# Kernel optimization log

Hardware: AMD Instinct MI355X
Metric: run time of the kernel (lower is better)

## Reference

```python
import jax, jax.numpy as jnp
import numpy as np

NEG_INF = -9e15
LEAKY_SLOPE = 0.2  # init alpha
N, IN_DIM, OUT_DIM = 8192, 512, 256


def setup_inputs() -> dict:
    key = jax.random.key(0)
    k1, k2, k3, k4, k5 = jax.random.split(key, 5)
    h = jax.random.normal(k1, (N, IN_DIM), dtype=jnp.float32)
    adj = jax.random.randint(k2, (N, N), 0, 2, dtype=jnp.int32)
    W = jax.random.normal(k3, (IN_DIM, OUT_DIM), dtype=jnp.float32) * 0.06
    a_left = jax.random.normal(k4, (OUT_DIM, 1), dtype=jnp.float32) * 0.1
    a_right = jax.random.normal(k5, (OUT_DIM, 1), dtype=jnp.float32) * 0.1
    return {"h": h, "adj": adj, "W": W, "a_left": a_left, "a_right": a_right}


def reference(h, adj, W, a_left, a_right):
    Wh = h @ W                                  # [N, out_dim]
    Wh1 = Wh @ a_left                           # [N, 1]
    Wh2 = Wh @ a_right                          # [N, 1]
    e = Wh1 + Wh2.T                             # [N, N] broadcast additive scores
    e = jnp.where(e > 0, e, LEAKY_SLOPE * e)    # LeakyReLU
    e = jnp.where(adj > 0, e, NEG_INF)          # adjacency mask
    attention = jax.nn.softmax(e, axis=1)       # row-wise softmax (dropout=0, eval)
    h_out = attention @ Wh                      # [N, out_dim]
    return jax.nn.elu(h_out)                    # activation=True
```

## Files before the change

kernel.cpp:

```cpp
#include <hip/hip_runtime.h>
#include <hip/hip_bf16.h>
#include <cstdint>
#include <cstddef>

typedef float  f32x4  __attribute__((ext_vector_type(4)));
typedef __bf16 bf16x8 __attribute__((ext_vector_type(8)));

#define LOG2E 1.4426950408889634f

static constexpr int GN   = 8192;
static constexpr int GIN  = 512;
static constexpr int GOUT = 256;

static __device__ __forceinline__ void gload_lds16(const void* g, void* lds){
  typedef uint32_t __attribute__((address_space(1)))* gp_t;
  typedef uint32_t __attribute__((address_space(3)))* lp_t;
  __builtin_amdgcn_global_load_lds((gp_t)(uintptr_t)g,
                                   (lp_t)(uint32_t)(uintptr_t)lds, 16, 0, 0);
}

__global__ __launch_bounds__(256) void k_pre1(const float* __restrict__ W,
                                              const float* __restrict__ al,
                                              const float* __restrict__ ar,
                                              const float* __restrict__ h,
                                              float* __restrict__ wal,
                                              float* __restrict__ war,
                                              __bf16* __restrict__ WT,
                                              __bf16* __restrict__ hb){
  __shared__ float T[64][65];
  const int bid = blockIdx.x, tid = threadIdx.x;
  if(bid < 128){
    const int k = bid*4 + (tid>>6), lane = tid & 63;
    float4 wv = ((const float4*)(W + (size_t)k*GOUT))[lane];
    float4 av = ((const float4*)al)[lane];
    float4 bv = ((const float4*)ar)[lane];
    float sl = wv.x*av.x + wv.y*av.y + wv.z*av.z + wv.w*av.w;
    float sr = wv.x*bv.x + wv.y*bv.y + wv.z*bv.z + wv.w*bv.w;
    #pragma unroll
    for(int o=32;o;o>>=1){ sl += __shfl_down(sl,o,64); sr += __shfl_down(sr,o,64); }
    if(lane==0){ wal[k] = sl*LOG2E; war[k] = sr*LOG2E; }
  } else if(bid < 160){
    const int tile = bid - 128;
    const int k0 = (tile>>2)*64, c0 = (tile&3)*64;
    const int r = tid>>2, cs = (tid&3)*16;
    #pragma unroll
    for(int j=0;j<4;j++){
      float4 v = *(const float4*)(W + (size_t)(k0+r)*GOUT + c0 + cs + 4*j);
      T[r][cs+4*j+0]=v.x; T[r][cs+4*j+1]=v.y; T[r][cs+4*j+2]=v.z; T[r][cs+4*j+3]=v.w;
    }
    __syncthreads();
    bf16x8 o1, o2;
    #pragma unroll
    for(int j=0;j<8;j++){ o1[j]=(__bf16)T[cs+j][r]; o2[j]=(__bf16)T[cs+8+j][r]; }
    __bf16* dst = WT + (size_t)(c0+r)*GIN + k0 + cs;
    *(bf16x8*)dst = o1;
    *(bf16x8*)(dst+8) = o2;
  } else {
    size_t i = ((size_t)(bid-160)*256 + tid)*8;
    float4 v0 = *(const float4*)(h+i);
    float4 v1 = *(const float4*)(h+i+4);
    bf16x8 o;
    o[0]=(__bf16)v0.x; o[1]=(__bf16)v0.y; o[2]=(__bf16)v0.z; o[3]=(__bf16)v0.w;
    o[4]=(__bf16)v1.x; o[5]=(__bf16)v1.y; o[6]=(__bf16)v1.z; o[7]=(__bf16)v1.w;
    *(bf16x8*)(hb+i) = o;
  }
}

__global__ __launch_bounds__(256) void k_pre2(const int* __restrict__ adj,
                                              unsigned int* __restrict__ pk,
                                              const __bf16* __restrict__ WT,
                                              const __bf16* __restrict__ hb,
                                              __bf16* __restrict__ WhbT,
                                              const float* __restrict__ h,
                                              const float* __restrict__ wal,
                                              const float* __restrict__ war,
                                              float* __restrict__ Wh1,
                                              float* __restrict__ Wh2){
  __shared__ __attribute__((aligned(16))) __bf16 As[2][64*64];
  __shared__ __attribute__((aligned(16))) __bf16 Bs[2][128*64];
  const int bid = blockIdx.x, tid = threadIdx.x;
  const int lane = tid & 63, w = tid >> 6;

  if(bid < 2048){
    const int Wv = bid*4 + w;
    const int jb = Wv & 127;
    const int g  = Wv >> 7;
    const size_t cb = (size_t)jb*64 + lane;
    const int idx = lane & 15;
    #pragma unroll 1
    for(int i=0;i<8;i++){
      const int r0 = (g*8 + i)*16;
      int a[16];
      #pragma unroll
      for(int r=0;r<16;r++) a[r] = adj[(size_t)(r0+r)*GN + cb];
      uint64_t b0 = __ballot(a[0]!=0),  b1 = __ballot(a[1]!=0);
      uint64_t b2 = __ballot(a[2]!=0),  b3 = __ballot(a[3]!=0);
      uint64_t b4 = __ballot(a[4]!=0),  b5 = __ballot(a[5]!=0);
      uint64_t b6 = __ballot(a[6]!=0),  b7 = __ballot(a[7]!=0);
      uint64_t b8 = __ballot(a[8]!=0),  b9 = __ballot(a[9]!=0);
      uint64_t bA = __ballot(a[10]!=0), bB = __ballot(a[11]!=0);
      uint64_t bC = __ballot(a[12]!=0), bD = __ballot(a[13]!=0);
      uint64_t bE = __ballot(a[14]!=0), bF = __ballot(a[15]!=0);
      uint64_t c0 = (idx&1)? b1:b0, c1 = (idx&1)? b3:b2;
      uint64_t c2 = (idx&1)? b5:b4, c3 = (idx&1)? b7:b6;
      uint64_t c4 = (idx&1)? b9:b8, c5 = (idx&1)? bB:bA;
      uint64_t c6 = (idx&1)? bD:bC, c7 = (idx&1)? bF:bE;
      uint64_t d0 = (idx&2)? c1:c0, d1 = (idx&2)? c3:c2;
      uint64_t d2 = (idx&2)? c5:c4, d3 = (idx&2)? c7:c6;
      uint64_t e0 = (idx&4)? d1:d0, e1 = (idx&4)? d3:d2;
      uint64_t v  = (idx&8)? e1:e0;
      unsigned int hword = (lane&16)? (unsigned int)(v>>32) : (unsigned int)v;
      if(lane < 32){
        pk[(size_t)(2*jb + (lane>>4))*GN + r0 + idx] = hword;
      }
    }
  } else if(bid < 2304){
    const int b2 = bid - 2048;
    const int mb = b2 >> 6, nb = b2 & 63;
    const int m0 = mb*64, n0 = nb*128;

    f32x4 acc[8];
    #pragma unroll
    for(int t=0;t<8;t++) acc[t] = (f32x4){0.f,0.f,0.f,0.f};

    const int lr = lane>>3;
    const int bs_sw = ((lane&7)*16) ^ (lr<<4);

    auto stage = [&](int it, int buf){
      const int k0b = it*128;
      #pragma unroll
      for(int s=0;s<6;s++){
        int u = w + s*4;
        const char* src; char* dst;
        if(u < 8){
          int r8 = u*8;
          src = (const char*)(WT + (size_t)(m0 + r8 + lr)*GIN);
          dst = (char*)&As[buf][0] + r8*128;
        } else {
          int r8 = (u-8)*8;
          src = (const char*)(hb + (size_t)(n0 + r8 + lr)*GIN);
          dst = (char*)&Bs[buf][0] + r8*128;
        }
        gload_lds16(src + k0b + bs_sw, dst);
      }
    };

    auto kstep = [&](int kk, int buf){
      const int ko = kk*64 + (lane>>4)*16;
      const int am = 16*w + (lane&15);
      bf16x8 af = *(const bf16x8*)((const char*)&As[buf][0] + am*128 + (ko ^ ((am&7)<<4)));
      #pragma unroll
      for(int t=0;t<8;t++){
        int n = 16*t + (lane&15);
        bf16x8 bf = *(const bf16x8*)((const char*)&Bs[buf][0] + n*128 + (ko ^ ((n&7)<<4)));
        acc[t] = __builtin_amdgcn_mfma_f32_16x16x32_bf16(af, bf, acc[t], 0, 0, 0);
      }
    };

    stage(0,0);
    asm volatile("s_waitcnt vmcnt(0)" ::: "memory");
    __builtin_amdgcn_s_barrier();
    for(int it=0; it<8; it++){
      int buf = it & 1;
      if(it < 7) stage(it+1, buf^1);
      kstep(0, buf);
      kstep(1, buf);
      asm volatile("s_waitcnt vmcnt(0)" ::: "memory");
      __builtin_amdgcn_s_barrier();
    }

    const int mrow = m0 + 16*w + 4*(lane>>4);
    const int nc0  = n0 + (lane&15);
    #pragma unroll
    for(int t=0;t<8;t++){
      #pragma unroll
      for(int r=0;r<4;r++){
        WhbT[(size_t)(mrow + r)*GN + nc0 + 16*t] = (__bf16)acc[t][r];
      }
    }
  } else {
    const int row = (bid-2304)*4 + w;
    const float4* hp = (const float4*)(h + (size_t)row*GIN);
    float4 v0 = hp[lane*2], v1 = hp[lane*2+1];
    float4 a0 = ((const float4*)wal)[lane*2], a1 = ((const float4*)wal)[lane*2+1];
    float4 b0 = ((const float4*)war)[lane*2], b1 = ((const float4*)war)[lane*2+1];
    float sl = v0.x*a0.x+v0.y*a0.y+v0.z*a0.z+v0.w*a0.w
             + v1.x*a1.x+v1.y*a1.y+v1.z*a1.z+v1.w*a1.w;
    float sr = v0.x*b0.x+v0.y*b0.y+v0.z*b0.z+v0.w*b0.w
             + v1.x*b1.x+v1.y*b1.y+v1.z*b1.z+v1.w*b1.w;
    #pragma unroll
    for(int of=32;of;of>>=1){ sl += __shfl_down(sl,of,64); sr += __shfl_down(sr,of,64); }
    if(lane==0){ Wh1[row]=sl; Wh2[row]=sr; }
  }
}

template<bool PART>
__global__ __launch_bounds__(256,2) void k_attn(const unsigned int* __restrict__ pk,
                                                const __bf16* __restrict__ WhbT,
                                                const float* __restrict__ Wh1s,
                                                const float* __restrict__ Wh2s,
                                                float* __restrict__ pv_out,
                                                float* __restrict__ s_out){
  __shared__ __attribute__((aligned(16))) char Vs[3][16384];
  const int tid = threadIdx.x, lane = tid & 63, w = tid >> 6;
  const int rg = blockIdx.x >> 3, chunk = blockIdx.x & 7;
  const int r0 = rg * 128;
  const int j0 = chunk * 1024;
  const int la = lane & 15, kg = lane >> 4, kg8 = kg << 3;

  f32x4 acc0[16], acc1[16];
  #pragma unroll
  for(int t=0;t<16;t++){ acc0[t] = (f32x4){0.f,0.f,0.f,0.f}; acc1[t] = (f32x4){0.f,0.f,0.f,0.f}; }
  f32x4 accs0 = (f32x4){0.f,0.f,0.f,0.f};
  f32x4 accs1 = (f32x4){0.f,0.f,0.f,0.f};

  bf16x8 ones;
  #pragma unroll
  for(int j=0;j<8;j++) ones[j] = (__bf16)1.0f;

  const int myrow0 = r0 + 16*w + la;
  const float wh1_0 = Wh1s[myrow0];
  const float wh1_1 = Wh1s[myrow0 + 64];

  const unsigned int* pkb = pk + (size_t)(chunk*32)*GN + r0 + 16*w + la;

  const int l_log = (lane&7) ^ (lane>>3);
  const char* wbase = (const char*)WhbT
                    + (size_t)(64*w + 2*(lane>>3) + (l_log>>2))*(GN*2)
                    + (size_t)(l_log&3)*16;

  auto stage = [&](int it, int buf){
    const size_t colb = (size_t)(j0 + it*32)*2;
    char* dst = &Vs[buf][0] + w*4096 + lane*16;
    #pragma unroll
    for(int s=0;s<4;s++){
      gload_lds16(wbase + (size_t)(16*s)*(GN*2) + colb, dst + s*1024);
    }
  };

  unsigned int mr0, mr1, nr0, nr1;
  auto mload = [&](int it, unsigned int& a, unsigned int& b){
    a = pkb[(size_t)it*GN];
    b = pkb[(size_t)it*GN + 64];
  };

  auto mkpa = [&](float wh1, unsigned m8, float4 w0, float4 w1) -> bf16x8 {
    bf16x8 pa;
    float y, p;
    y = wh1 + w0.x; y = fmaxf(y, 0.2f*y); p = exp2f(y); pa[0] = (__bf16)((m8    )&1 ? p : 0.f);
    y = wh1 + w0.y; y = fmaxf(y, 0.2f*y); p = exp2f(y); pa[1] = (__bf16)((m8>>1)&1 ? p : 0.f);
    y = wh1 + w0.z; y = fmaxf(y, 0.2f*y); p = exp2f(y); pa[2] = (__bf16)((m8>>2)&1 ? p : 0.f);
    y = wh1 + w0.w; y = fmaxf(y, 0.2f*y); p = exp2f(y); pa[3] = (__bf16)((m8>>3)&1 ? p : 0.f);
    y = wh1 + w1.x; y = fmaxf(y, 0.2f*y); p = exp2f(y); pa[4] = (__bf16)((m8>>4)&1 ? p : 0.f);
    y = wh1 + w1.y; y = fmaxf(y, 0.2f*y); p = exp2f(y); pa[5] = (__bf16)((m8>>5)&1 ? p : 0.f);
    y = wh1 + w1.z; y = fmaxf(y, 0.2f*y); p = exp2f(y); pa[6] = (__bf16)((m8>>6)&1 ? p : 0.f);
    y = wh1 + w1.w; y = fmaxf(y, 0.2f*y); p = exp2f(y); pa[7] = (__bf16)((m8>>7)&1 ? p : 0.f);
    return pa;
  };

  const int rd_off = (la>>1)*128 + (((((la&1)<<2) | kg) ^ (la>>1)) << 4);

  auto kstep = [&](int it, int buf){
    const float* wp = Wh2s + j0 + it*32 + kg8;
    float4 w0 = *(const float4*)wp;
    float4 w1 = *(const float4*)(wp + 4);
    bf16x8 pa0 = mkpa(wh1_0, (mr0 >> kg8) & 0xffu, w0, w1);
    bf16x8 pa1 = mkpa(wh1_1, (mr1 >> kg8) & 0xffu, w0, w1);
    const char* vb = &Vs[buf][0] + rd_off;
    #pragma unroll
    for(int t=0;t<16;t++){
      bf16x8 bv = *(const bf16x8*)(vb + t*1024);
      acc0[t] = __builtin_amdgcn_mfma_f32_16x16x32_bf16(pa0, bv, acc0[t], 0, 0, 0);
      acc1[t] = __builtin_amdgcn_mfma_f32_16x16x32_bf16(pa1, bv, acc1[t], 0, 0, 0);
    }
    accs0 = __builtin_amdgcn_mfma_f32_16x16x32_bf16(pa0, ones, accs0, 0, 0, 0);
    accs1 = __builtin_amdgcn_mfma_f32_16x16x32_bf16(pa1, ones, accs1, 0, 0, 0);
  };

  mload(0, mr0, mr1);
  stage(0, 0);
  stage(1, 1);
  asm volatile("s_waitcnt vmcnt(4)" ::: "memory");
  __builtin_amdgcn_s_barrier();

  for(int it=0; it<32; it++){
    const int buf = it % 3;
    if(it < 31) mload(it+1, nr0, nr1);
    if(it < 30) stage(it+2, (it+2)%3);
    kstep(it, buf);
    mr0 = nr0; mr1 = nr1;
    if(it < 30){
      asm volatile("s_waitcnt vmcnt(6)" ::: "memory");
      __builtin_amdgcn_s_barrier();
    } else if(it == 30){
      asm volatile("s_waitcnt vmcnt(2)" ::: "memory");
      __builtin_amdgcn_s_barrier();
    }
  }

  const int orow0 = r0 + 16*w + 4*kg;
  const int orow1 = orow0 + 64;
  const int ocol  = la;
  if constexpr (PART){
    float* pv = pv_out + (size_t)chunk*GN*GOUT;
    float* sp = s_out  + (size_t)chunk*GN;
    #pragma unroll
    for(int t=0;t<16;t++){
      #pragma unroll
      for(int r=0;r<4;r++){
        pv[(size_t)(orow0 + r)*GOUT + ocol + 16*t] = acc0[t][r];
        pv[(size_t)(orow1 + r)*GOUT + ocol + 16*t] = acc1[t][r];
      }
    }
    if(ocol == 0){
      #pragma unroll
      for(int r=0;r<4;r++){ sp[orow0 + r] = accs0[r]; sp[orow1 + r] = accs1[r]; }
    }
  } else {
    #pragma unroll
    for(int t=0;t<16;t++){
      #pragma unroll
      for(int r=0;r<4;r++){
        atomicAdd(pv_out + (size_t)(orow0 + r)*GOUT + ocol + 16*t, acc0[t][r]);
        atomicAdd(pv_out + (size_t)(orow1 + r)*GOUT + ocol + 16*t, acc1[t][r]);
      }
    }
    if(ocol == 0){
      #pragma unroll
      for(int r=0;r<4;r++){ atomicAdd(s_out + orow0 + r, accs0[r]); atomicAdd(s_out + orow1 + r, accs1[r]); }
    }
  }
}

static __device__ __forceinline__ float elu1(float x){
  return x > 0.f ? x : (exp2f(x*LOG2E) - 1.f);
}

__global__ void k_reduce(const float* __restrict__ accP, const float* __restrict__ accSp,
                         float* __restrict__ out){
  size_t i = ((size_t)blockIdx.x*256 + threadIdx.x)*4;
  int row = (int)(i >> 8);
  float S = 0.f;
  #pragma unroll
  for(int c=0;c<8;c++) S += accSp[(size_t)c*GN + row];
  float4 s = {0.f,0.f,0.f,0.f};
  #pragma unroll
  for(int c=0;c<8;c++){
    float4 v = *(const float4*)(accP + (size_t)c*GN*GOUT + i);
    s.x += v.x; s.y += v.y; s.z += v.z; s.w += v.w;
  }
  float inv = 1.0f / S;
  float4 o;
  o.x = elu1(s.x*inv); o.y = elu1(s.y*inv); o.z = elu1(s.z*inv); o.w = elu1(s.w*inv);
  *(float4*)(out + i) = o;
}

__global__ void k_norm(const float* __restrict__ accPV, const float* __restrict__ accS,
                       float* __restrict__ out){
  size_t i = ((size_t)blockIdx.x*256 + threadIdx.x)*4;
  int row = (int)(i >> 8);
  float inv = 1.0f / accS[row];
  float4 v = *(const float4*)(accPV + i);
  float4 o;
  o.x = elu1(v.x*inv); o.y = elu1(v.y*inv); o.z = elu1(v.z*inv); o.w = elu1(v.w*inv);
  *(float4*)(out + i) = o;
}

extern "C" void kernel_launch(void* const* d_in, const int* in_sizes, int n_in,
                              void* d_out, int out_size, void* d_ws, size_t ws_size,
                              hipStream_t stream){
  const float* h  = (const float*)d_in[0];
  const int*   adj= (const int*)  d_in[1];
  const float* W  = (const float*)d_in[2];
  const float* al = (const float*)d_in[3];
  const float* ar = (const float*)d_in[4];
  float* out = (float*)d_out;
  char* ws = (char*)d_ws;

  const size_t SZ_ACCP = (size_t)8*GN*GOUT*4;
  const size_t SZ_PK   = (size_t)256*GN*4;
  const size_t NEED_A  = SZ_ACCP + 4194304 + 32768 + 32768 + 262144 + SZ_PK;

  if(ws_size >= NEED_A){
    float*  accP  = (float*) (ws);
    __bf16* hb    = (__bf16*)(ws);
    __bf16* WT    = (__bf16*)(ws + 8388608);
    float*  wal   = (float*) (ws + 8650752);
    float*  war   = (float*) (ws + 8652800);
    __bf16* WhbT  = (__bf16*)(ws + SZ_ACCP);
    float*  Wh1   = (float*) (ws + SZ_ACCP + 4194304);
    float*  Wh2   = (float*) (ws + SZ_ACCP + 4227072);
    float*  accSp = (float*) (ws + SZ_ACCP + 4259840);
    unsigned int* pk = (unsigned int*)(ws + SZ_ACCP + 4521984);

    k_pre1<<<2208, 256, 0, stream>>>(W, al, ar, h, wal, war, WT, hb);
    k_pre2<<<4352, 256, 0, stream>>>(adj, pk, WT, hb, WhbT, h, wal, war, Wh1, Wh2);
    k_attn<true><<<512, 256, 0, stream>>>(pk, WhbT, Wh1, Wh2, accP, accSp);
    k_reduce<<<2048, 256, 0, stream>>>(accP, accSp, out);
  } else {
    float*  accPV = (float*) (ws);
    float*  accS  = (float*) (ws + 8388608);
    __bf16* hb    = (__bf16*)(ws + 8421376);
    __bf16* WT    = (__bf16*)(ws + 16809984);
    __bf16* WhbT  = (__bf16*)(ws + 17072128);
    float*  wal   = (float*) (ws + 21266432);
    float*  war   = (float*) (ws + 21268480);
    float*  Wh1   = (float*) (ws + 21270528);
    float*  Wh2   = (float*) (ws + 21303296);
    unsigned int* pk = (unsigned int*)(ws + 21336064);
    if(ws_size < 21336064 + SZ_PK) return;

    hipMemsetAsync(accPV, 0, 8388608 + 32768, stream);
    k_pre1<<<2208, 256, 0, stream>>>(W, al, ar, h, wal, war, WT, hb);
    k_pre2<<<4352, 256, 0, stream>>>(adj, pk, WT, hb, WhbT, h, wal, war, Wh1, Wh2);
    k_attn<false><<<512, 256, 0, stream>>>(pk, WhbT, Wh1, Wh2, accPV, accS);
    k_norm<<<2048, 256, 0, stream>>>(accPV, accS, out);
  }
}
```

Before: 144.6 us.

## Preload adjacency mask and Wh2 into LDS, switch V staging to double buffering

The block's whole 32x128 packed adjacency-mask tile and its 1024 Wh2 values are loaded into shared memory once at kernel start. Each k-step then reads them from LDS instead of issuing per-iteration global loads. The V tile pipeline drops from three LDS buffers to two, and every iteration waits with vmcnt(0) before the barrier. This removes small scattered global loads from the inner loop, but it shortens the prefetch distance and raises LDS use per block, which may expose more memory latency.

```diff
diff --git a/kernel.cpp b/kernel.cpp
--- a/kernel.cpp
+++ b/kernel.cpp
@@ -201,48 +201,55 @@
                                                 const float* __restrict__ Wh2s,
                                                 float* __restrict__ pv_out,
                                                 float* __restrict__ s_out){
-  __shared__ __attribute__((aligned(16))) char Vs[3][16384];
+  __shared__ __attribute__((aligned(16))) char Vs[2][16384];
+  __shared__ __attribute__((aligned(16))) unsigned int mkL[32*128];
+  __shared__ __attribute__((aligned(16))) float wh2L[1024];
   const int tid = threadIdx.x, lane = tid & 63, w = tid >> 6;
   const int rg = blockIdx.x >> 3, chunk = blockIdx.x & 7;
   const int r0 = rg * 128;
   const int j0 = chunk * 1024;
   const int la = lane & 15, kg = lane >> 4, kg8 = kg << 3;
 
+  const int jrow = tid >> 5, c4 = (tid & 31) * 4;
+  uint4 mv0 = *(const uint4*)(pk + (size_t)(chunk*32 +  0 + jrow)*GN + r0 + c4);
+  uint4 mv1 = *(const uint4*)(pk + (size_t)(chunk*32 +  8 + jrow)*GN + r0 + c4);
+  uint4 mv2 = *(const uint4*)(pk + (size_t)(chunk*32 + 16 + jrow)*GN + r0 + c4);
+  uint4 mv3 = *(const uint4*)(pk + (size_t)(chunk*32 + 24 + jrow)*GN + r0 + c4);
+  float4 wv = *(const float4*)(Wh2s + j0 + tid*4);
+  const float wh1_0 = Wh1s[r0 + 16*w + la];
+  const float wh1_1 = Wh1s[r0 + 16*w + la + 64];
+
+  const int l_log = (lane&7) ^ (lane>>3);
+  const char* wbase = (const char*)WhbT
+                    + (size_t)(64*w + 2*(lane>>3) + (l_log>>2))*(GN*2)
+                    + (size_t)(l_log&3)*16;
+  auto stage = [&](int it, int buf){
+    const size_t colb = (size_t)(j0 + it*32)*2;
+    char* dst = &Vs[buf][0] + w*4096 + lane*16;
+    #pragma unroll
+    for(int s=0;s<4;s++){
+      gload_lds16(wbase + (size_t)(16*s)*(GN*2) + colb, dst + s*1024);
+    }
+  };
+
+  stage(0, 0);
+
+  *(uint4*)&mkL[( 0 + jrow)*128 + c4] = mv0;
+  *(uint4*)&mkL[( 8 + jrow)*128 + c4] = mv1;
+  *(uint4*)&mkL[(16 + jrow)*128 + c4] = mv2;
+  *(uint4*)&mkL[(24 + jrow)*128 + c4] = mv3;
+  *(float4*)&wh2L[tid*4] = wv;
+
   f32x4 acc0[16], acc1[16];
   #pragma unroll
   for(int t=0;t<16;t++){ acc0[t] = (f32x4){0.f,0.f,0.f,0.f}; acc1[t] = (f32x4){0.f,0.f,0.f,0.f}; }
   f32x4 accs0 = (f32x4){0.f,0.f,0.f,0.f};
   f32x4 accs1 = (f32x4){0.f,0.f,0.f,0.f};
-
   bf16x8 ones;
   #pragma unroll
   for(int j=0;j<8;j++) ones[j] = (__bf16)1.0f;
 
-  const int myrow0 = r0 + 16*w + la;
-  const float wh1_0 = Wh1s[myrow0];
-  const float wh1_1 = Wh1s[myrow0 + 64];
-
-  const unsigned int* pkb = pk + (size_t)(chunk*32)*GN + r0 + 16*w + la;
-
-  const int l_log = (lane&7) ^ (lane>>3);
-  const char* wbase = (const char*)WhbT
-                    + (size_t)(64*w + 2*(lane>>3) + (l_log>>2))*(GN*2)
-                    + (size_t)(l_log&3)*16;
-
-  auto stage = [&](int it, int buf){
-    const size_t colb = (size_t)(j0 + it*32)*2;
-    char* dst = &Vs[buf][0] + w*4096 + lane*16;
-    #pragma unroll
-    for(int s=0;s<4;s++){
-      gload_lds16(wbase + (size_t)(16*s)*(GN*2) + colb, dst + s*1024);
-    }
-  };
-
-  unsigned int mr0, mr1, nr0, nr1;
-  auto mload = [&](int it, unsigned int& a, unsigned int& b){
-    a = pkb[(size_t)it*GN];
-    b = pkb[(size_t)it*GN + 64];
-  };
+  __syncthreads();
 
   auto mkpa = [&](float wh1, unsigned m8, float4 w0, float4 w1) -> bf16x8 {
     bf16x8 pa;
@@ -261,11 +268,13 @@
   const int rd_off = (la>>1)*128 + (((((la&1)<<2) | kg) ^ (la>>1)) << 4);
 
   auto kstep = [&](int it, int buf){
-    const float* wp = Wh2s + j0 + it*32 + kg8;
+    unsigned int m0 = mkL[it*128 + 16*w + la];
+    unsigned int m1 = mkL[it*128 + 16*w + la + 64];
+    const float* wp = &wh2L[it*32 + kg8];
     float4 w0 = *(const float4*)wp;
     float4 w1 = *(const float4*)(wp + 4);
-    bf16x8 pa0 = mkpa(wh1_0, (mr0 >> kg8) & 0xffu, w0, w1);
-    bf16x8 pa1 = mkpa(wh1_1, (mr1 >> kg8) & 0xffu, w0, w1);
+    bf16x8 pa0 = mkpa(wh1_0, (m0 >> kg8) & 0xffu, w0, w1);
+    bf16x8 pa1 = mkpa(wh1_1, (m1 >> kg8) & 0xffu, w0, w1);
     const char* vb = &Vs[buf][0] + rd_off;
     #pragma unroll
     for(int t=0;t<16;t++){
@@ -277,25 +286,12 @@
     accs1 = __builtin_amdgcn_mfma_f32_16x16x32_bf16(pa1, ones, accs1, 0, 0, 0);
   };
 
-  mload(0, mr0, mr1);
-  stage(0, 0);
-  stage(1, 1);
-  asm volatile("s_waitcnt vmcnt(4)" ::: "memory");
-  __builtin_amdgcn_s_barrier();
-
   for(int it=0; it<32; it++){
-    const int buf = it % 3;
-    if(it < 31) mload(it+1, nr0, nr1);
-    if(it < 30) stage(it+2, (it+2)%3);
+    const int buf = it & 1;
+    if(it < 31) stage(it+1, buf^1);
     kstep(it, buf);
-    mr0 = nr0; mr1 = nr1;
-    if(it < 30){
-      asm volatile("s_waitcnt vmcnt(6)" ::: "memory");
-      __builtin_amdgcn_s_barrier();
-    } else if(it == 30){
-      asm volatile("s_waitcnt vmcnt(2)" ::: "memory");
-      __builtin_amdgcn_s_barrier();
-    }
+    asm volatile("s_waitcnt vmcnt(0)" ::: "memory");
+    __builtin_amdgcn_s_barrier();
   }
 
   const int orow0 = r0 + 16*w + 4*kg;
```

After: 141.5 us. 1.02x faster.
